# Optimization experiments

Hardware: AMD Instinct MI355X
Metric: run time of the kernel (lower is better)

## Reference

```python
import jax, jax.numpy as jnp
import numpy as np

N_EXPERTS = 8
N_SHARED = 1
N_ROUTED = N_EXPERTS - N_SHARED          # 7
TOP_K_ROUTED = 3 - N_SHARED              # 2 routed experts per token
C = 1024
H = 4 * C


def _mlp(x, w_fc, w_proj):
    # x: [n, C]; w_fc: [C, H]; w_proj: [H, C]; exact (erf) GELU like torch nn.GELU
    return jax.nn.gelu(x @ w_fc, approximate=False) @ w_proj


def setup_inputs() -> dict:
    key = jax.random.key(0)
    ks = jax.random.split(key, 6)
    s = 0.02
    return {
        "x": jax.random.normal(ks[0], (4, 2048, C), dtype=jnp.float32),
        "gate_w": jax.random.normal(ks[1], (N_ROUTED, C), dtype=jnp.float32) * s,
        "lb_bias": jnp.zeros((N_ROUTED,), dtype=jnp.float32),
        "shared_wfc": jax.random.normal(ks[2], (C, H), dtype=jnp.float32) * s,
        "shared_wproj": jax.random.normal(ks[3], (H, C), dtype=jnp.float32) * s,
        "routed_wfc": jax.random.normal(ks[4], (N_ROUTED, C, H), dtype=jnp.float32) * s,
        "routed_wproj": jax.random.normal(ks[5], (N_ROUTED, H, C), dtype=jnp.float32) * s,
    }


def reference(x, gate_w, lb_bias, shared_wfc, shared_wproj, routed_wfc, routed_wproj):
    B, T, Cc = x.shape
    xt = x.reshape(-1, Cc)                       # [n, C]
    n = xt.shape[0]

    # shared expert(s) applied to every token
    shared_out = _mlp(xt, shared_wfc, shared_wproj)

    # routing
    routed_logits = xt @ gate_w.T                # [n, E_r]
    sel_logits = routed_logits + lb_bias
    _, topk_idx = jax.lax.top_k(sel_logits, TOP_K_ROUTED)   # [n, k]
    routed_probs = jax.nn.softmax(routed_logits.astype(jnp.float32), axis=-1)
    topk_w = jnp.take_along_axis(routed_probs, topk_idx, axis=-1)  # [n, k]

    # per-token combine weights over routed experts: [n, E_r]
    cw = jnp.zeros((n, N_ROUTED), dtype=jnp.float32)
    cw = cw.at[jnp.arange(n)[:, None], topk_idx].add(topk_w)

    # dispatch-combine: small fixed loop over routed experts
    routed_out = jnp.zeros_like(xt)
    for e in range(N_ROUTED):
        y = _mlp(xt, routed_wfc[e], routed_wproj[e])
        routed_out = routed_out + cw[:, e:e + 1] * y

    return (shared_out + routed_out).reshape(B, T, Cc)
```

## Files before the change

### kernel.cpp

```cpp
#include <hip/hip_runtime.h>
#include <hip/hip_bf16.h>

#define AS1 __attribute__((address_space(1)))
#define AS3 __attribute__((address_space(3)))

typedef __bf16 bf16x8 __attribute__((ext_vector_type(8)));
typedef float f32x4 __attribute__((ext_vector_type(4)));

static constexpr int C_DIM = 1024;
static constexpr int H_DIM = 4096;
static constexpr int NTOK  = 8192;
static constexpr int NR    = 7;
static constexpr int NSLOT = 17408;
static constexpr int MAXIDX = 17664;
static constexpr int MAXT  = 72;
static constexpr size_t WSZ = (size_t)C_DIM * H_DIM;

static __device__ __forceinline__ unsigned short f2bf(float f) {
  __hip_bfloat16 h = __float2bfloat16(f);
  return *reinterpret_cast<unsigned short*>(&h);
}
static __device__ __forceinline__ float bf2f(unsigned short u) {
  unsigned int v = ((unsigned int)u) << 16;
  return *reinterpret_cast<float*>(&v);
}

static __device__ __forceinline__ void gload16(const void* g, void* lds) {
  __builtin_amdgcn_global_load_lds((const AS1 void*)g, (AS3 void*)lds, 16, 0, 0);
}

__global__ __launch_bounds__(256) void cast_x_kernel(const float* __restrict__ x,
                                                     unsigned short* __restrict__ xb) {
  size_t i = ((size_t)blockIdx.x * blockDim.x + threadIdx.x) * 4;
  float4 v = *(const float4*)(x + i);
  ushort4 o;
  o.x = f2bf(v.x); o.y = f2bf(v.y); o.z = f2bf(v.z); o.w = f2bf(v.w);
  *(ushort4*)(xb + i) = o;
}

__global__ __launch_bounds__(256) void init_kernel(int* __restrict__ idx, int* __restrict__ cnt,
                                                   int* __restrict__ cursor) {
  int i = blockIdx.x * 256 + threadIdx.x;
  if (i < MAXIDX) idx[i] = 0;
  if (blockIdx.x == 0 && threadIdx.x < 8) { cnt[threadIdx.x] = 0; cursor[threadIdx.x] = 0; }
}

__global__ __launch_bounds__(256) void routing_kernel(const float* __restrict__ x,
                                                      const float* __restrict__ gw,
                                                      const float* __restrict__ bias,
                                                      float* __restrict__ cw,
                                                      int* __restrict__ cnt) {
  int wid = (int)((blockIdx.x * (size_t)blockDim.x + threadIdx.x) >> 6);
  int lane = threadIdx.x & 63;
  if (wid >= NTOK) return;
  const float* xt = x + (size_t)wid * C_DIM;
  float p[NR] = {0.f, 0.f, 0.f, 0.f, 0.f, 0.f, 0.f};
  for (int i = lane; i < C_DIM; i += 64) {
    float xv = xt[i];
#pragma unroll
    for (int e = 0; e < NR; ++e) p[e] += xv * gw[e * C_DIM + i];
  }
#pragma unroll
  for (int e = 0; e < NR; ++e) {
#pragma unroll
    for (int off = 32; off; off >>= 1) p[e] += __shfl_down(p[e], off);
  }
  if (lane == 0) {
    float m = p[0];
#pragma unroll
    for (int e = 1; e < NR; ++e) m = fmaxf(m, p[e]);
    float pr[NR], s = 0.f;
#pragma unroll
    for (int e = 0; e < NR; ++e) { pr[e] = __expf(p[e] - m); s += pr[e]; }
    float inv = 1.0f / s;
#pragma unroll
    for (int e = 0; e < NR; ++e) pr[e] *= inv;
    float sel[NR];
#pragma unroll
    for (int e = 0; e < NR; ++e) sel[e] = p[e] + bias[e];
    int i1 = 0;
#pragma unroll
    for (int e = 1; e < NR; ++e) if (sel[e] > sel[i1]) i1 = e;
    int i2 = -1;
#pragma unroll
    for (int e = 0; e < NR; ++e) {
      if (e == i1) continue;
      if (i2 < 0 || sel[e] > sel[i2]) i2 = e;
    }
    float c[NR] = {0.f, 0.f, 0.f, 0.f, 0.f, 0.f, 0.f};
    c[i1] = pr[i1];
    c[i2] += pr[i2];
#pragma unroll
    for (int e = 0; e < NR; ++e) cw[(size_t)wid * NR + e] = c[e];
    atomicAdd(&cnt[i1], 1);
    atomicAdd(&cnt[i2], 1);
  }
}

__global__ void scan_kernel(const int* __restrict__ cnt, int* __restrict__ offs,
                            int* __restrict__ tmap, int* __restrict__ tlim,
                            int* __restrict__ ntiles) {
  int o = 0, nt = 0;
  for (int e = 0; e < NR; ++e) {
    offs[e] = o;
    int a = (cnt[e] + 127) & ~127;
    for (int tm = 0; tm < a; tm += 256) {
      tmap[nt] = ((e + 1) << 20) | (o + tm);
      tlim[nt] = o + a;
      ++nt;
    }
    o += a;
  }
  *ntiles = nt;
}

__global__ __launch_bounds__(256) void place_kernel(const float* __restrict__ cw,
                                                    const int* __restrict__ offs,
                                                    int* __restrict__ cursor,
                                                    int* __restrict__ idx,
                                                    int* __restrict__ tok2slot,
                                                    float* __restrict__ tok2w) {
  int t = blockIdx.x * 256 + threadIdx.x;
  if (t >= NTOK) return;
  int k = 0;
#pragma unroll
  for (int e = 0; e < NR; ++e) {
    float w = cw[(size_t)t * NR + e];
    if (w > 0.f) {
      int p = atomicAdd(&cursor[e], 1);
      int slot = offs[e] + p;
      idx[slot] = t;
      tok2slot[t * 2 + k] = slot;
      tok2w[t * 2 + k] = w;
      ++k;
    }
  }
}

__global__ void transpose_cast_all(const float* __restrict__ shared_w,
                                   const float* __restrict__ routed_w,
                                   unsigned short* __restrict__ out, int R, int S) {
  int e = blockIdx.z;
  const float* in = (e == 0) ? shared_w : routed_w + (size_t)(e - 1) * R * S;
  unsigned short* o = out + (size_t)e * R * S;
  __shared__ float t[32][33];
  int bx = blockIdx.x * 32;
  int by = blockIdx.y * 32;
  int tx = threadIdx.x, ty = threadIdx.y;
#pragma unroll
  for (int i = 0; i < 32; i += 8)
    t[ty + i][tx] = in[(size_t)(by + ty + i) * S + bx + tx];
  __syncthreads();
#pragma unroll
  for (int i = 0; i < 32; i += 8)
    o[(size_t)(bx + ty + i) * R + by + tx] = f2bf(t[tx][ty + i]);
}

template <int EPI, bool GATHER, int K, int NSPLIT>
__global__ __launch_bounds__(512, 2) void gemm256(const unsigned short* __restrict__ A,
                                                  const unsigned short* __restrict__ BtAll,
                                                  unsigned short* __restrict__ Ybf,
                                                  unsigned short* __restrict__ Pb,
                                                  const int* __restrict__ idx,
                                                  const int* __restrict__ tmap,
                                                  const int* __restrict__ tlim,
                                                  const int* __restrict__ ntiles) {
  __shared__ __align__(16) unsigned short As[2][8192];
  __shared__ __align__(16) unsigned short Bs[2][8192];
  constexpr int KSEG = K / NSPLIT;
  constexpr int NT = KSEG / 32;
  const int tid = threadIdx.x;
  const int wave = tid >> 6, lane = tid & 63;
  const int kbase = blockIdx.z * KSEG;

  int m0, lim;
  const unsigned short* Bt;
  if (GATHER) {
    if (blockIdx.y >= *ntiles) return;
    const int packed = tmap[blockIdx.y];
    m0 = packed & 0xfffff;
    lim = tlim[blockIdx.y];
    Bt = BtAll + (size_t)(packed >> 20) * WSZ;
  } else {
    m0 = blockIdx.y * 256;
    lim = 1 << 30;
    Bt = BtAll;
  }
  const int n0 = blockIdx.x * 256;

  const int kg = tid >> 8;
  const int r  = tid & 255;
  int arow = m0 + r;
  if (EPI == 0 && GATHER) arow = idx[arow];
  const unsigned short* gA = A + (size_t)arow * K + kbase;
  const unsigned short* gB = Bt + (size_t)(n0 + r) * K + kbase;
  const int gA0off = kg * 8, gA1off = (kg + 2) * 8;
  const int d0 = (wave >> 2) * 2048 + (wave & 3) * 512;
  const int d1 = d0 + 4096;

  const int wr = wave >> 2, wc = wave & 3;
  const int fr = lane & 15, fq = lane >> 4;
  f32x4 acc[8][4] = {};

  asm volatile("s_waitcnt vmcnt(0)" ::: "memory");
  gload16(gA + gA0off, &As[0][d0]);
  gload16(gA + gA1off, &As[0][d1]);
  gload16(gB + gA0off, &Bs[0][d0]);
  gload16(gB + gA1off, &Bs[0][d1]);

  int rb = 0;
  for (int t = 0; t < NT; ++t) {
    if (t + 1 < NT) {
      const int wb = rb ^ 1;
      const int nk = (t + 1) * 32;
      gload16(gA + nk + gA0off, &As[wb][d0]);
      gload16(gA + nk + gA1off, &As[wb][d1]);
      gload16(gB + nk + gA0off, &Bs[wb][d0]);
      gload16(gB + nk + gA1off, &Bs[wb][d1]);
      asm volatile("s_waitcnt vmcnt(4)" ::: "memory");
    } else {
      asm volatile("s_waitcnt vmcnt(0)" ::: "memory");
    }
    __builtin_amdgcn_s_barrier();
    bf16x8 af[8], bfr[4];
#pragma unroll
    for (int m = 0; m < 8; ++m)
      af[m] = *(const bf16x8*)&As[rb][fq * 2048 + (wr * 128 + m * 16 + fr) * 8];
#pragma unroll
    for (int n = 0; n < 4; ++n)
      bfr[n] = *(const bf16x8*)&Bs[rb][fq * 2048 + (wc * 64 + n * 16 + fr) * 8];
#pragma unroll
    for (int m = 0; m < 8; ++m)
#pragma unroll
      for (int n = 0; n < 4; ++n)
        acc[m][n] = __builtin_amdgcn_mfma_f32_16x16x32_bf16(af[m], bfr[n], acc[m][n], 0, 0, 0);
    __builtin_amdgcn_s_barrier();
    rb ^= 1;
  }

#pragma unroll
  for (int m = 0; m < 8; ++m)
#pragma unroll
    for (int n = 0; n < 4; ++n)
#pragma unroll
      for (int j = 0; j < 4; ++j) {
        const int slot = m0 + wr * 128 + m * 16 + fq * 4 + j;
        const int col = n0 + wc * 64 + n * 16 + fr;
        const float v = acc[m][n][j];
        if (EPI == 0) {
          if (!GATHER || slot < lim) {
            const float g = 0.5f * v * (1.0f + erff(v * 0.70710678118654752f));
            Ybf[(size_t)slot * H_DIM + col] = f2bf(g);
          }
        } else {
          if (slot < lim)
            Pb[((size_t)blockIdx.z * NSLOT + slot) * C_DIM + col] = f2bf(v);
        }
      }
}

__global__ __launch_bounds__(256) void gemm_proj_shared(const unsigned short* __restrict__ Yg,
                                                        const unsigned short* __restrict__ Bt,
                                                        float* __restrict__ Out) {
  __shared__ __align__(16) unsigned short As[3][4096];
  __shared__ __align__(16) unsigned short Bs[3][4096];
  const int tid = threadIdx.x;
  const int wave = tid >> 6, lane = tid & 63;
  constexpr int NT = H_DIM / 32;

  const int f = blockIdx.y * gridDim.x + blockIdx.x;
  const int cpx = (gridDim.x * gridDim.y) >> 3;
  const int swz = (f & 7) * cpx + (f >> 3);
  const int m0 = (swz / gridDim.x) * 128;
  const int n0 = (swz % gridDim.x) * 128;

  const int q0 = wave * 128 + lane, q1 = q0 + 64;
  const int kg0 = q0 >> 7, r0 = q0 & 127;
  const int kg1 = q1 >> 7, r1 = q1 & 127;
  const unsigned short* gA0 = Yg + (size_t)(m0 + r0) * H_DIM + kg0 * 8;
  const unsigned short* gA1 = Yg + (size_t)(m0 + r1) * H_DIM + kg1 * 8;
  const unsigned short* gB0 = Bt + (size_t)(n0 + r0) * H_DIM + kg0 * 8;
  const unsigned short* gB1 = Bt + (size_t)(n0 + r1) * H_DIM + kg1 * 8;
  const int c0 = (wave * 2 + 0) * 512, c1 = (wave * 2 + 1) * 512;

  const int wr = wave >> 1, wc = wave & 1;
  const int fr = lane & 15, fq = lane >> 4;
  f32x4 acc[4][4] = {};

  gload16(gA0, &As[0][c0]); gload16(gA1, &As[0][c1]);
  gload16(gB0, &Bs[0][c0]); gload16(gB1, &Bs[0][c1]);
  gload16(gA0 + 32, &As[1][c0]); gload16(gA1 + 32, &As[1][c1]);
  gload16(gB0 + 32, &Bs[1][c0]); gload16(gB1 + 32, &Bs[1][c1]);

  int rb = 0;
  for (int t = 0; t < NT; ++t) {
    if (t + 2 < NT) {
      const int wb = (rb >= 1) ? rb - 1 : 2;
      const int nk = (t + 2) * 32;
      gload16(gA0 + nk, &As[wb][c0]); gload16(gA1 + nk, &As[wb][c1]);
      gload16(gB0 + nk, &Bs[wb][c0]); gload16(gB1 + nk, &Bs[wb][c1]);
      asm volatile("s_waitcnt vmcnt(8)" ::: "memory");
    } else if (t + 1 < NT) {
      asm volatile("s_waitcnt vmcnt(4)" ::: "memory");
    } else {
      asm volatile("s_waitcnt vmcnt(0)" ::: "memory");
    }
    __builtin_amdgcn_s_barrier();
    bf16x8 af[4], bfr[4];
#pragma unroll
    for (int m = 0; m < 4; ++m)
      af[m] = *(const bf16x8*)&As[rb][fq * 1024 + (wr * 64 + m * 16 + fr) * 8];
#pragma unroll
    for (int n = 0; n < 4; ++n)
      bfr[n] = *(const bf16x8*)&Bs[rb][fq * 1024 + (wc * 64 + n * 16 + fr) * 8];
#pragma unroll
    for (int m = 0; m < 4; ++m)
#pragma unroll
      for (int n = 0; n < 4; ++n)
        acc[m][n] = __builtin_amdgcn_mfma_f32_16x16x32_bf16(af[m], bfr[n], acc[m][n], 0, 0, 0);
    __builtin_amdgcn_s_barrier();
    rb = (rb == 2) ? 0 : rb + 1;
  }

#pragma unroll
  for (int m = 0; m < 4; ++m)
#pragma unroll
    for (int n = 0; n < 4; ++n)
#pragma unroll
      for (int j = 0; j < 4; ++j) {
        const int p = wr * 64 + m * 16 + fq * 4 + j;
        const int col = n0 + wc * 64 + n * 16 + fr;
        Out[(size_t)(m0 + p) * C_DIM + col] = acc[m][n][j];
      }
}

__global__ __launch_bounds__(256) void combine_kernel(const unsigned short* __restrict__ P,
                                                      const int* __restrict__ tok2slot,
                                                      const float* __restrict__ tok2w,
                                                      float* __restrict__ out) {
  const int t = blockIdx.x;
  const int c = threadIdx.x * 4;
  const int s0 = tok2slot[t * 2], s1 = tok2slot[t * 2 + 1];
  const float w0 = tok2w[t * 2], w1 = tok2w[t * 2 + 1];
  const ushort4 a0 = *(const ushort4*)&P[((size_t)0 * NSLOT + s0) * C_DIM + c];
  const ushort4 a1 = *(const ushort4*)&P[((size_t)1 * NSLOT + s0) * C_DIM + c];
  const ushort4 b0 = *(const ushort4*)&P[((size_t)0 * NSLOT + s1) * C_DIM + c];
  const ushort4 b1 = *(const ushort4*)&P[((size_t)1 * NSLOT + s1) * C_DIM + c];
  float4 o = *(float4*)&out[(size_t)t * C_DIM + c];
  o.x += w0 * (bf2f(a0.x) + bf2f(a1.x)) + w1 * (bf2f(b0.x) + bf2f(b1.x));
  o.y += w0 * (bf2f(a0.y) + bf2f(a1.y)) + w1 * (bf2f(b0.y) + bf2f(b1.y));
  o.z += w0 * (bf2f(a0.z) + bf2f(a1.z)) + w1 * (bf2f(b0.z) + bf2f(b1.z));
  o.w += w0 * (bf2f(a0.w) + bf2f(a1.w)) + w1 * (bf2f(b0.w) + bf2f(b1.w));
  *(float4*)&out[(size_t)t * C_DIM + c] = o;
}

extern "C" void kernel_launch(void* const* d_in, const int* in_sizes, int n_in,
                              void* d_out, int out_size, void* d_ws, size_t ws_size,
                              hipStream_t stream) {
  const float* x            = (const float*)d_in[0];
  const float* gate_w       = (const float*)d_in[1];
  const float* lb_bias      = (const float*)d_in[2];
  const float* shared_wfc   = (const float*)d_in[3];
  const float* shared_wproj = (const float*)d_in[4];
  const float* routed_wfc   = (const float*)d_in[5];
  const float* routed_wproj = (const float*)d_in[6];
  float* out = (float*)d_out;

  char* ws = (char*)d_ws;
  unsigned short* xb     = (unsigned short*)(ws);
  unsigned short* wfcT   = (unsigned short*)(ws + 16777216);
  unsigned short* Pb     = (unsigned short*)(ws);
  unsigned short* wprojT = (unsigned short*)(ws + 83886080);
  unsigned short* Yg     = (unsigned short*)(ws + 150994944);
  float*          cw     = (float*)(ws + 293601280);
  int*            idx    = (int*)(ws + 293830656);
  int*            cnt    = (int*)(ws + 293901312);
  int*            offs   = (int*)(ws + 293901376);
  int*            cursor = (int*)(ws + 293901440);
  int*            tok2slot = (int*)(ws + 293901504);
  float*          tok2w    = (float*)(ws + 293967040);
  int*            tmap     = (int*)(ws + 294032576);
  int*            tlim     = (int*)(ws + 294032864);
  int*            ntiles   = (int*)(ws + 294033152);

  cast_x_kernel<<<NTOK * C_DIM / (256 * 4), 256, 0, stream>>>(x, xb);
  init_kernel<<<(MAXIDX + 255) / 256, 256, 0, stream>>>(idx, cnt, cursor);
  routing_kernel<<<NTOK / 4, 256, 0, stream>>>(x, gate_w, lb_bias, cw, cnt);
  scan_kernel<<<1, 1, 0, stream>>>(cnt, offs, tmap, tlim, ntiles);
  place_kernel<<<NTOK / 256, 256, 0, stream>>>(cw, offs, cursor, idx, tok2slot, tok2w);

  transpose_cast_all<<<dim3(H_DIM / 32, C_DIM / 32, 8), dim3(32, 8), 0, stream>>>(
      shared_wfc, routed_wfc, wfcT, C_DIM, H_DIM);
  transpose_cast_all<<<dim3(C_DIM / 32, H_DIM / 32, 8), dim3(32, 8), 0, stream>>>(
      shared_wproj, routed_wproj, wprojT, H_DIM, C_DIM);

  gemm256<0, false, C_DIM, 1><<<dim3(H_DIM / 256, NTOK / 256), 512, 0, stream>>>(
      xb, wfcT, Yg, nullptr, idx, tmap, tlim, ntiles);
  gemm_proj_shared<<<dim3(C_DIM / 128, NTOK / 128), 256, 0, stream>>>(Yg, wprojT, out);

  gemm256<0, true, C_DIM, 1><<<dim3(H_DIM / 256, MAXT), 512, 0, stream>>>(
      xb, wfcT, Yg, nullptr, idx, tmap, tlim, ntiles);
  gemm256<2, true, H_DIM, 2><<<dim3(C_DIM / 256, MAXT, 2), 512, 0, stream>>>(
      Yg, wprojT, nullptr, Pb, idx, tmap, tlim, ntiles);

  combine_kernel<<<NTOK, 256, 0, stream>>>(Pb, tok2slot, tok2w, out);
}
```

Before: 1.402 ms.

## Rewrite expert GEMMs as 256x256 ping-pong quadrant pipeline with fast GELU

Replaces the gemm256 kernel with gemm256ph. It uses K-tiles of 64, splits the 256x256 tile into four 128-quadrant phases and interleaves half-tile global-to-LDS loads between phases, with s_setprio around MFMA bursts. GELU moves from erf to a tanh-style exp/rcp approximation. The shared projection GEMM gets a grouped XCD-aware tile swizzle, projection outputs use nontemporal stores, and MAXT grows to 76 with workspace offsets shifted to match. The aim is better overlap of memory and MFMA and cheaper epilogues. The trade-offs are fewer resident blocks (launch bounds now allow 1 block per CU, LDS doubled) and an approximate GELU that may change accuracy.

```diff
diff --git a/kernel.cpp b/kernel.cpp
--- a/kernel.cpp
+++ b/kernel.cpp
@@ -13,7 +13,7 @@
 static constexpr int NR    = 7;
 static constexpr int NSLOT = 17408;
 static constexpr int MAXIDX = 17664;
-static constexpr int MAXT  = 72;
+static constexpr int MAXT  = 76;
 static constexpr size_t WSZ = (size_t)C_DIM * H_DIM;
 
 static __device__ __forceinline__ unsigned short f2bf(float f) {
@@ -25,8 +25,28 @@
   return *reinterpret_cast<float*>(&v);
 }
 
+static __device__ __forceinline__ float gelu_fast(float v) {
+  const float u2 = -2.0f * v * (0.7978845608f + 0.0356774081f * v * v);
+  return v * __builtin_amdgcn_rcpf(1.0f + __expf(u2));
+}
+
 static __device__ __forceinline__ void gload16(const void* g, void* lds) {
   __builtin_amdgcn_global_load_lds((const AS1 void*)g, (AS3 void*)lds, 16, 0, 0);
+}
+
+static __device__ __forceinline__ void tile_decode(int f, int gx, int gy,
+                                                   int& ty, int& bx) {
+  const int myc = gy >> 3;
+  const int xcd = f & 7;
+  const int r = f >> 3;
+  const int GM = 8;
+  const int nig = GM * gx;
+  const int grp = r / nig;
+  const int first = grp * GM;
+  const int gsz = min(GM, myc - first);
+  const int rin = r - grp * nig;
+  ty = xcd * myc + first + rin % gsz;
+  bx = rin / gsz;
 }
 
 __global__ __launch_bounds__(256) void cast_x_kernel(const float* __restrict__ x,
@@ -156,26 +176,25 @@
     o[(size_t)(bx + ty + i) * R + by + tx] = f2bf(t[tx][ty + i]);
 }
 
-template <int EPI, bool GATHER, int K, int NSPLIT>
-__global__ __launch_bounds__(512, 2) void gemm256(const unsigned short* __restrict__ A,
-                                                  const unsigned short* __restrict__ BtAll,
-                                                  unsigned short* __restrict__ Ybf,
-                                                  unsigned short* __restrict__ Pb,
-                                                  const int* __restrict__ idx,
-                                                  const int* __restrict__ tmap,
-                                                  const int* __restrict__ tlim,
-                                                  const int* __restrict__ ntiles) {
-  __shared__ __align__(16) unsigned short As[2][8192];
-  __shared__ __align__(16) unsigned short Bs[2][8192];
-  constexpr int KSEG = K / NSPLIT;
-  constexpr int NT = KSEG / 32;
+template <int EPI, bool TMAPPED, bool AIDX, int K, int LDA>
+__global__ __launch_bounds__(512, 1) void gemm256ph(const unsigned short* __restrict__ A,
+                                                    const unsigned short* __restrict__ BtAll,
+                                                    unsigned short* __restrict__ Yout,
+                                                    unsigned short* __restrict__ Pb,
+                                                    const int* __restrict__ idx,
+                                                    const int* __restrict__ tmap,
+                                                    const int* __restrict__ tlim,
+                                                    const int* __restrict__ ntiles) {
+  __shared__ __align__(16) unsigned short As[2][2][8192];
+  __shared__ __align__(16) unsigned short Bs[2][2][8192];
+  constexpr int NT = K / 64;
   const int tid = threadIdx.x;
-  const int wave = tid >> 6, lane = tid & 63;
-  const int kbase = blockIdx.z * KSEG;
+  const int w = tid >> 6, lane = tid & 63;
+  const int kbase = blockIdx.z * K;
 
   int m0, lim;
   const unsigned short* Bt;
-  if (GATHER) {
+  if (TMAPPED) {
     if (blockIdx.y >= *ntiles) return;
     const int packed = tmap[blockIdx.y];
     m0 = packed & 0xfffff;
@@ -188,75 +207,146 @@
   }
   const int n0 = blockIdx.x * 256;
 
-  const int kg = tid >> 8;
-  const int r  = tid & 255;
-  int arow = m0 + r;
-  if (EPI == 0 && GATHER) arow = idx[arow];
-  const unsigned short* gA = A + (size_t)arow * K + kbase;
-  const unsigned short* gB = Bt + (size_t)(n0 + r) * K + kbase;
-  const int gA0off = kg * 8, gA1off = (kg + 2) * 8;
-  const int d0 = (wave >> 2) * 2048 + (wave & 3) * 512;
-  const int d1 = d0 + 4096;
-
-  const int wr = wave >> 2, wc = wave & 3;
+  const unsigned short* aptr[2][2];
+  const unsigned short* bptr[2][2];
+#pragma unroll
+  for (int h = 0; h < 2; ++h)
+#pragma unroll
+    for (int j = 0; j < 2; ++j) {
+      int slot = m0 + h * 128 + j * 64 + lane;
+      size_t arow = AIDX ? (size_t)idx[slot] : (size_t)slot;
+      aptr[h][j] = A + arow * LDA + kbase + w * 8;
+      bptr[h][j] = Bt + (size_t)(n0 + h * 128 + j * 64 + lane) * LDA + kbase + w * 8;
+    }
+  const int w1024 = w * 1024;
+
+#define STG_A(b, h, T)                                              \
+  do {                                                              \
+    gload16(aptr[h][0] + (size_t)(T) * 64, &As[b][h][w1024]);       \
+    gload16(aptr[h][1] + (size_t)(T) * 64, &As[b][h][w1024 + 512]); \
+  } while (0)
+#define STG_B(b, h, T)                                              \
+  do {                                                              \
+    gload16(bptr[h][0] + (size_t)(T) * 64, &Bs[b][h][w1024]);       \
+    gload16(bptr[h][1] + (size_t)(T) * 64, &Bs[b][h][w1024 + 512]); \
+  } while (0)
+
   const int fr = lane & 15, fq = lane >> 4;
-  f32x4 acc[8][4] = {};
+  const int ar = (w >> 2) * 64;
+  const int bc = (w & 3) * 32;
+
+  f32x4 acc[4][4][2] = {};
 
   asm volatile("s_waitcnt vmcnt(0)" ::: "memory");
-  gload16(gA + gA0off, &As[0][d0]);
-  gload16(gA + gA1off, &As[0][d1]);
-  gload16(gB + gA0off, &Bs[0][d0]);
-  gload16(gB + gA1off, &Bs[0][d1]);
-
-  int rb = 0;
+  STG_A(0, 0, 0); STG_B(0, 0, 0); STG_A(0, 1, 0); STG_B(0, 1, 0);
+  STG_A(1, 0, 1); STG_B(1, 0, 1);
+
   for (int t = 0; t < NT; ++t) {
-    if (t + 1 < NT) {
-      const int wb = rb ^ 1;
-      const int nk = (t + 1) * 32;
-      gload16(gA + nk + gA0off, &As[wb][d0]);
-      gload16(gA + nk + gA1off, &As[wb][d1]);
-      gload16(gB + nk + gA0off, &Bs[wb][d0]);
-      gload16(gB + nk + gA1off, &Bs[wb][d1]);
-      asm volatile("s_waitcnt vmcnt(4)" ::: "memory");
-    } else {
-      asm volatile("s_waitcnt vmcnt(0)" ::: "memory");
-    }
-    __builtin_amdgcn_s_barrier();
-    bf16x8 af[8], bfr[4];
-#pragma unroll
-    for (int m = 0; m < 8; ++m)
-      af[m] = *(const bf16x8*)&As[rb][fq * 2048 + (wr * 128 + m * 16 + fr) * 8];
-#pragma unroll
-    for (int n = 0; n < 4; ++n)
-      bfr[n] = *(const bf16x8*)&Bs[rb][fq * 2048 + (wc * 64 + n * 16 + fr) * 8];
-#pragma unroll
-    for (int m = 0; m < 8; ++m)
-#pragma unroll
-      for (int n = 0; n < 4; ++n)
-        acc[m][n] = __builtin_amdgcn_mfma_f32_16x16x32_bf16(af[m], bfr[n], acc[m][n], 0, 0, 0);
-    __builtin_amdgcn_s_barrier();
-    rb ^= 1;
-  }
-
-#pragma unroll
-  for (int m = 0; m < 8; ++m)
-#pragma unroll
-    for (int n = 0; n < 4; ++n)
-#pragma unroll
-      for (int j = 0; j < 4; ++j) {
-        const int slot = m0 + wr * 128 + m * 16 + fq * 4 + j;
-        const int col = n0 + wc * 64 + n * 16 + fr;
-        const float v = acc[m][n][j];
-        if (EPI == 0) {
-          if (!GATHER || slot < lim) {
-            const float g = 0.5f * v * (1.0f + erff(v * 0.70710678118654752f));
-            Ybf[(size_t)slot * H_DIM + col] = f2bf(g);
+    const int r = t & 1, wb = r ^ 1;
+    bf16x8 af[4][2], b0[2][2], b1[2][2];
+
+    if (t + 1 < NT) STG_A(wb, 1, t + 1);
+    if (t == NT - 1) asm volatile("s_waitcnt vmcnt(4)" ::: "memory");
+    else             asm volatile("s_waitcnt vmcnt(8)" ::: "memory");
+    __builtin_amdgcn_s_barrier();
+#pragma unroll
+    for (int m = 0; m < 4; ++m)
+#pragma unroll
+      for (int ks = 0; ks < 2; ++ks)
+        af[m][ks] = *(const bf16x8*)&As[r][0][(ks * 4 + fq) * 1024 + (ar + m * 16 + fr) * 8];
+#pragma unroll
+    for (int n = 0; n < 2; ++n)
+#pragma unroll
+      for (int ks = 0; ks < 2; ++ks)
+        b0[n][ks] = *(const bf16x8*)&Bs[r][0][(ks * 4 + fq) * 1024 + (bc + n * 16 + fr) * 8];
+    __builtin_amdgcn_s_setprio(1);
+#pragma unroll
+    for (int m = 0; m < 4; ++m)
+#pragma unroll
+      for (int n = 0; n < 2; ++n)
+#pragma unroll
+        for (int ks = 0; ks < 2; ++ks)
+          acc[0][m][n] = __builtin_amdgcn_mfma_f32_16x16x32_bf16(af[m][ks], b0[n][ks], acc[0][m][n], 0, 0, 0);
+    __builtin_amdgcn_s_setprio(0);
+    __builtin_amdgcn_s_barrier();
+
+    if (t + 1 < NT) STG_B(wb, 1, t + 1);
+    if (t == NT - 1) asm volatile("s_waitcnt vmcnt(0)" ::: "memory");
+    else             asm volatile("s_waitcnt vmcnt(6)" ::: "memory");
+    __builtin_amdgcn_s_barrier();
+#pragma unroll
+    for (int n = 0; n < 2; ++n)
+#pragma unroll
+      for (int ks = 0; ks < 2; ++ks)
+        b1[n][ks] = *(const bf16x8*)&Bs[r][1][(ks * 4 + fq) * 1024 + (bc + n * 16 + fr) * 8];
+    __builtin_amdgcn_s_setprio(1);
+#pragma unroll
+    for (int m = 0; m < 4; ++m)
+#pragma unroll
+      for (int n = 0; n < 2; ++n)
+#pragma unroll
+        for (int ks = 0; ks < 2; ++ks)
+          acc[1][m][n] = __builtin_amdgcn_mfma_f32_16x16x32_bf16(af[m][ks], b1[n][ks], acc[1][m][n], 0, 0, 0);
+    __builtin_amdgcn_s_setprio(0);
+    __builtin_amdgcn_s_barrier();
+
+    if (t + 2 < NT) STG_A(r, 0, t + 2);
+    __builtin_amdgcn_s_barrier();
+#pragma unroll
+    for (int m = 0; m < 4; ++m)
+#pragma unroll
+      for (int ks = 0; ks < 2; ++ks)
+        af[m][ks] = *(const bf16x8*)&As[r][1][(ks * 4 + fq) * 1024 + (ar + m * 16 + fr) * 8];
+    __builtin_amdgcn_s_setprio(1);
+#pragma unroll
+    for (int m = 0; m < 4; ++m)
+#pragma unroll
+      for (int n = 0; n < 2; ++n)
+#pragma unroll
+        for (int ks = 0; ks < 2; ++ks)
+          acc[2][m][n] = __builtin_amdgcn_mfma_f32_16x16x32_bf16(af[m][ks], b1[n][ks], acc[2][m][n], 0, 0, 0);
+    __builtin_amdgcn_s_setprio(0);
+    __builtin_amdgcn_s_barrier();
+
+    if (t + 2 < NT) STG_B(r, 0, t + 2);
+    __builtin_amdgcn_s_barrier();
+    __builtin_amdgcn_s_setprio(1);
+#pragma unroll
+    for (int m = 0; m < 4; ++m)
+#pragma unroll
+      for (int n = 0; n < 2; ++n)
+#pragma unroll
+        for (int ks = 0; ks < 2; ++ks)
+          acc[3][m][n] = __builtin_amdgcn_mfma_f32_16x16x32_bf16(af[m][ks], b0[n][ks], acc[3][m][n], 0, 0, 0);
+    __builtin_amdgcn_s_setprio(0);
+    __builtin_amdgcn_s_barrier();
+  }
+#undef STG_A
+#undef STG_B
+
+#pragma unroll
+  for (int q = 0; q < 4; ++q) {
+    const int hm = q >> 1;
+    const int hn = (q == 1 || q == 2) ? 1 : 0;
+#pragma unroll
+    for (int m = 0; m < 4; ++m)
+#pragma unroll
+      for (int n = 0; n < 2; ++n)
+#pragma unroll
+        for (int j = 0; j < 4; ++j) {
+          const int slot = m0 + hm * 128 + ar + m * 16 + fq * 4 + j;
+          const int col = n0 + hn * 128 + bc + n * 16 + fr;
+          const float v = acc[q][m][n][j];
+          if (EPI == 0) {
+            if (!TMAPPED || slot < lim)
+              Yout[(size_t)slot * H_DIM + col] = f2bf(gelu_fast(v));
+          } else {
+            if (slot < lim)
+              __builtin_nontemporal_store(
+                  f2bf(v), &Pb[((size_t)blockIdx.z * NSLOT + slot) * C_DIM + col]);
           }
-        } else {
-          if (slot < lim)
-            Pb[((size_t)blockIdx.z * NSLOT + slot) * C_DIM + col] = f2bf(v);
         }
-      }
+  }
 }
 
 __global__ __launch_bounds__(256) void gemm_proj_shared(const unsigned short* __restrict__ Yg,
@@ -268,11 +358,13 @@
   const int wave = tid >> 6, lane = tid & 63;
   constexpr int NT = H_DIM / 32;
 
-  const int f = blockIdx.y * gridDim.x + blockIdx.x;
-  const int cpx = (gridDim.x * gridDim.y) >> 3;
-  const int swz = (f & 7) * cpx + (f >> 3);
-  const int m0 = (swz / gridDim.x) * 128;
-  const int n0 = (swz % gridDim.x) * 128;
+  int bx, ty;
+  {
+    const int f = blockIdx.y * gridDim.x + blockIdx.x;
+    tile_decode(f, gridDim.x, gridDim.y, ty, bx);
+  }
+  const int m0 = ty * 128;
+  const int n0 = bx * 128;
 
   const int q0 = wave * 128 + lane, q1 = q0 + 64;
   const int kg0 = q0 >> 7, r0 = q0 & 127;
@@ -380,8 +472,8 @@
   int*            tok2slot = (int*)(ws + 293901504);
   float*          tok2w    = (float*)(ws + 293967040);
   int*            tmap     = (int*)(ws + 294032576);
-  int*            tlim     = (int*)(ws + 294032864);
-  int*            ntiles   = (int*)(ws + 294033152);
+  int*            tlim     = (int*)(ws + 294032960);
+  int*            ntiles   = (int*)(ws + 294033344);
 
   cast_x_kernel<<<NTOK * C_DIM / (256 * 4), 256, 0, stream>>>(x, xb);
   init_kernel<<<(MAXIDX + 255) / 256, 256, 0, stream>>>(idx, cnt, cursor);
@@ -394,13 +486,13 @@
   transpose_cast_all<<<dim3(C_DIM / 32, H_DIM / 32, 8), dim3(32, 8), 0, stream>>>(
       shared_wproj, routed_wproj, wprojT, H_DIM, C_DIM);
 
-  gemm256<0, false, C_DIM, 1><<<dim3(H_DIM / 256, NTOK / 256), 512, 0, stream>>>(
+  gemm256ph<0, false, false, C_DIM, C_DIM><<<dim3(H_DIM / 256, NTOK / 256, 1), 512, 0, stream>>>(
       xb, wfcT, Yg, nullptr, idx, tmap, tlim, ntiles);
   gemm_proj_shared<<<dim3(C_DIM / 128, NTOK / 128), 256, 0, stream>>>(Yg, wprojT, out);
 
-  gemm256<0, true, C_DIM, 1><<<dim3(H_DIM / 256, MAXT), 512, 0, stream>>>(
+  gemm256ph<0, true, true, C_DIM, C_DIM><<<dim3(H_DIM / 256, MAXT, 1), 512, 0, stream>>>(
       xb, wfcT, Yg, nullptr, idx, tmap, tlim, ntiles);
-  gemm256<2, true, H_DIM, 2><<<dim3(C_DIM / 256, MAXT, 2), 512, 0, stream>>>(
+  gemm256ph<2, true, false, H_DIM / 2, H_DIM><<<dim3(C_DIM / 256, MAXT, 2), 512, 0, stream>>>(
       Yg, wprojT, nullptr, Pb, idx, tmap, tlim, ntiles);
 
   combine_kernel<<<NTOK, 256, 0, stream>>>(Pb, tok2slot, tok2w, out);
```

New measurement: 1.287 ms. -8.2%, faster.
